# Optimization experiments

Hardware: AMD Instinct MI355X
Metric: run time of the kernel (lower is better)

Reference implementation:

```python
import jax, jax.numpy as jnp
import numpy as np

N = 8192
F_IN = 256
F_OUT = 128
ALPHA = 0.2  # leaky relu negative slope


def _leaky(x):
    return jnp.where(x >= 0, x, ALPHA * x)


def setup_inputs() -> dict:
    key = jax.random.key(0)
    ks = jax.random.split(key, 12)
    nodes = jax.random.normal(ks[0], (N, F_IN), dtype=jnp.float32)
    adj = (jax.random.uniform(ks[1], (N, N)) < 0.05).astype(jnp.float32)
    adj = jnp.maximum(adj, jnp.eye(N, dtype=jnp.float32))
    s = 0.02
    W1 = jax.random.normal(ks[2], (F_IN, F_OUT), dtype=jnp.float32) * s
    b1 = jnp.zeros((F_OUT,), jnp.float32)
    W2 = jax.random.normal(ks[3], (F_OUT, F_OUT), dtype=jnp.float32) * s
    b2 = jnp.zeros((F_OUT,), jnp.float32)
    W3 = jax.random.normal(ks[4], (F_OUT, F_OUT), dtype=jnp.float32) * s
    b3 = jnp.zeros((F_OUT,), jnp.float32)
    W4 = jax.random.normal(ks[5], (F_OUT, F_OUT), dtype=jnp.float32) * s
    b4 = jnp.zeros((F_OUT,), jnp.float32)
    a_w = jax.random.normal(ks[6], (2 * F_OUT,), dtype=jnp.float32) * s
    a_b = jnp.zeros((), jnp.float32)
    return {"nodes": nodes, "adj": adj, "W1": W1, "b1": b1, "W2": W2, "b2": b2,
            "W3": W3, "b3": b3, "W4": W4, "b4": b4, "a_w": a_w, "a_b": a_b}


def reference(nodes, adj, W1, b1, W2, b2, W3, b3, W4, b4, a_w, a_b):
    # 4-layer linear stack
    h = jax.nn.relu(nodes @ W1 + b1)
    h = jax.nn.relu(h @ W2 + b2)
    h = jax.nn.relu(h @ W3 + b3)
    h = h @ W4 + b4  # (N, F_OUT)
    # a([h_i, h_j]) is linear -> split into src/dst components instead of
    # materializing the (N, N, 2F) repeat+cat tensor; identical math.
    a1, a2 = a_w[:F_OUT], a_w[F_OUT:]
    s_src = h @ a1  # (N,)
    s_dst = h @ a2  # (N,)
    e = _leaky(s_src[:, None] + s_dst[None, :] + a_b)  # (N, N)
    e = jnp.where(adj >= 0.5, e, -jnp.inf)
    attention = jax.nn.softmax(e, axis=1)
    # dropout is identity in eval mode
    return _leaky(attention @ h)  # (N, F_OUT)
```

## Files before the change

### kernel.cpp

```cpp
#include <hip/hip_runtime.h>
#include <hip/hip_bf16.h>

#define N_NODES 8192
#define F_IN    256
#define F_OUT   128
#define BM      16
#define CHUNK   512
#define NCH     4
#define CCAP    768

typedef float f4v __attribute__((ext_vector_type(4)));
typedef unsigned int u32;

__device__ __forceinline__ float leaky(float x) { return x >= 0.f ? x : 0.2f * x; }
__device__ __forceinline__ u32 bf16rn(float a) {
  const u32 u = __float_as_uint(a);
  return (u + 0x7FFFu + ((u >> 16) & 1u)) >> 16;
}
__device__ __forceinline__ u32 packbf(float a, float b) {
  return bf16rn(a) | (bf16rn(b) << 16);
}
__device__ __forceinline__ float bflo(u32 u) { return __uint_as_float(u << 16); }
__device__ __forceinline__ float bfhi(u32 u) { return __uint_as_float(u & 0xFFFF0000u); }

__global__ __launch_bounds__(256) void mlp_fused(
    const float* __restrict__ nodes,
    const float* __restrict__ W1, const float* __restrict__ b1,
    const float* __restrict__ W2, const float* __restrict__ b2,
    const float* __restrict__ W3, const float* __restrict__ b3,
    const float* __restrict__ W4, const float* __restrict__ b4,
    const float* __restrict__ aw,
    u32* __restrict__ hb_out, float* __restrict__ ss, float* __restrict__ sd) {
  __shared__ float As[32][18];
  __shared__ float Ws[32][128];
  __shared__ float hTa[128][18];
  __shared__ float hTb[128][18];
  __shared__ float awS[2 * F_OUT];
  __shared__ float sred[2][16][16];

  const int tid = threadIdx.x;
  const int bm0 = blockIdx.x * BM;
  const int mt = tid >> 5;
  const int nt = tid & 31;

  awS[tid] = aw[tid];

  float acc[2][4] = {};

  const bool al = tid < 128;
  const int ar = tid >> 3;
  const int ac = tid & 7;
  for (int k0 = 0; k0 < F_IN; k0 += 32) {
    float4 av;
    if (al) av = *(const float4*)(nodes + (size_t)(bm0 + ar) * F_IN + k0 + ac * 4);
    float4 wv[4];
#pragma unroll
    for (int i = 0; i < 4; ++i) {
      const int kk = i * 8 + mt;
      wv[i] = *(const float4*)(W1 + (size_t)(k0 + kk) * F_OUT + nt * 4);
    }
    __syncthreads();
    if (al) {
      As[ac * 4 + 0][ar] = av.x;
      As[ac * 4 + 1][ar] = av.y;
      As[ac * 4 + 2][ar] = av.z;
      As[ac * 4 + 3][ar] = av.w;
    }
#pragma unroll
    for (int i = 0; i < 4; ++i) *(float4*)&Ws[i * 8 + mt][nt * 4] = wv[i];
    __syncthreads();
#pragma unroll
    for (int k = 0; k < 32; ++k) {
      const float2 a = *(const float2*)&As[k][mt * 2];
      const float4 w = *(const float4*)&Ws[k][nt * 4];
      acc[0][0] += a.x * w.x; acc[0][1] += a.x * w.y; acc[0][2] += a.x * w.z; acc[0][3] += a.x * w.w;
      acc[1][0] += a.y * w.x; acc[1][1] += a.y * w.y; acc[1][2] += a.y * w.z; acc[1][3] += a.y * w.w;
    }
  }
  {
    const float4 bv = *(const float4*)(b1 + nt * 4);
#pragma unroll
    for (int i = 0; i < 2; ++i) {
      hTa[nt * 4 + 0][mt * 2 + i] = fmaxf(acc[i][0] + bv.x, 0.f);
      hTa[nt * 4 + 1][mt * 2 + i] = fmaxf(acc[i][1] + bv.y, 0.f);
      hTa[nt * 4 + 2][mt * 2 + i] = fmaxf(acc[i][2] + bv.z, 0.f);
      hTa[nt * 4 + 3][mt * 2 + i] = fmaxf(acc[i][3] + bv.w, 0.f);
    }
  }

  const float* Wl[3] = {W2, W3, W4};
  const float* bl[3] = {b2, b3, b4};
  float* hin = &hTa[0][0];
  float* hout = &hTb[0][0];
  for (int l = 0; l < 3; ++l) {
#pragma unroll
    for (int i = 0; i < 2; ++i)
#pragma unroll
      for (int j = 0; j < 4; ++j) acc[i][j] = 0.f;
    for (int k0 = 0; k0 < F_OUT; k0 += 32) {
      float4 wv[4];
#pragma unroll
      for (int i = 0; i < 4; ++i) {
        const int kk = i * 8 + mt;
        wv[i] = *(const float4*)(Wl[l] + (size_t)(k0 + kk) * F_OUT + nt * 4);
      }
      __syncthreads();
#pragma unroll
      for (int i = 0; i < 4; ++i) *(float4*)&Ws[i * 8 + mt][nt * 4] = wv[i];
      __syncthreads();
#pragma unroll
      for (int k = 0; k < 32; ++k) {
        const float2 a = *(const float2*)(hin + (size_t)(k0 + k) * 18 + mt * 2);
        const float4 w = *(const float4*)&Ws[k][nt * 4];
        acc[0][0] += a.x * w.x; acc[0][1] += a.x * w.y; acc[0][2] += a.x * w.z; acc[0][3] += a.x * w.w;
        acc[1][0] += a.y * w.x; acc[1][1] += a.y * w.y; acc[1][2] += a.y * w.z; acc[1][3] += a.y * w.w;
      }
    }
    const float4 bv = *(const float4*)(bl[l] + nt * 4);
    const bool relu = (l < 2);
#pragma unroll
    for (int i = 0; i < 2; ++i) {
      float o0 = acc[i][0] + bv.x, o1 = acc[i][1] + bv.y;
      float o2 = acc[i][2] + bv.z, o3 = acc[i][3] + bv.w;
      if (relu) {
        o0 = fmaxf(o0, 0.f); o1 = fmaxf(o1, 0.f);
        o2 = fmaxf(o2, 0.f); o3 = fmaxf(o3, 0.f);
      }
      hout[(size_t)(nt * 4 + 0) * 18 + mt * 2 + i] = o0;
      hout[(size_t)(nt * 4 + 1) * 18 + mt * 2 + i] = o1;
      hout[(size_t)(nt * 4 + 2) * 18 + mt * 2 + i] = o2;
      hout[(size_t)(nt * 4 + 3) * 18 + mt * 2 + i] = o3;
    }
    float* t = hin; hin = hout; hout = t;
  }
  __syncthreads();

  {
    const int r = tid & 15;
    const int fg = tid >> 4;
    float s1 = 0.f, s2 = 0.f;
#pragma unroll
    for (int i = 0; i < 8; ++i) {
      const int f = fg * 8 + i;
      const float hv = hin[(size_t)f * 18 + r];
      s1 += hv * awS[f];
      s2 += hv * awS[F_OUT + f];
    }
    sred[0][fg][r] = s1;
    sred[1][fg][r] = s2;
  }
  {
    const int r = tid >> 4;
    const int c = tid & 15;
    const int f0 = c * 8;
    uint4 o;
    o.x = packbf(hin[(size_t)(f0 + 0) * 18 + r], hin[(size_t)(f0 + 1) * 18 + r]);
    o.y = packbf(hin[(size_t)(f0 + 2) * 18 + r], hin[(size_t)(f0 + 3) * 18 + r]);
    o.z = packbf(hin[(size_t)(f0 + 4) * 18 + r], hin[(size_t)(f0 + 5) * 18 + r]);
    o.w = packbf(hin[(size_t)(f0 + 6) * 18 + r], hin[(size_t)(f0 + 7) * 18 + r]);
    ((uint4*)hb_out)[(size_t)(bm0 + r) * 16 + c] = o;
  }
  __syncthreads();
  if (tid < 16) {
    float s1 = 0.f, s2 = 0.f;
#pragma unroll
    for (int g = 0; g < 16; ++g) { s1 += sred[0][g][tid]; s2 += sred[1][g][tid]; }
    ss[bm0 + tid] = s1;
    sd[bm0 + tid] = s2;
  }
}

__global__ __launch_bounds__(512) void attn_kernel(const float* __restrict__ adj,
                                                   const u32* __restrict__ hb,
                                                   const float* __restrict__ s_src,
                                                   const float* __restrict__ s_dst,
                                                   const float* __restrict__ ab_ptr,
                                                   float* __restrict__ out) {
  __shared__ float2 lst[2][CCAP];
  __shared__ int   cnt[NCH];
  __shared__ float accs[32][16][8];
  __shared__ float red_sum[8];

  const int tid = threadIdx.x;
  const int lane = tid & 63;
  const int wid = tid >> 6;
  const int row = blockIdx.x;
  if (tid < NCH) cnt[tid] = 0;

  const float sbase = s_src[row] + ab_ptr[0];
  const f4v* arow = (const f4v*)(adj + (size_t)row * N_NODES);
  const float4* sd4 = (const float4*)s_dst;
  const uint4* hb4 = (const uint4*)hb;
  const unsigned long long lt = (1ull << lane) - 1ull;
  const int g = tid >> 4;
  const int q = tid & 15;

  f4v av = __builtin_nontemporal_load(arow + tid);
  float4 sv = sd4[tid];

  float lsum = 0.f;
  float accv[8] = {};
  __syncthreads();

#pragma unroll
  for (int c = 0; c < NCH; ++c) {
    const f4v av_c = av;
    const float4 sv_c = sv;
    if (c + 1 < NCH) {
      av = __builtin_nontemporal_load(arow + (c + 1) * CHUNK + tid);
      sv = sd4[(c + 1) * CHUNK + tid];
    }
    const bool hx = av_c.x >= 0.5f, hy = av_c.y >= 0.5f, hz = av_c.z >= 0.5f, hw = av_c.w >= 0.5f;
    const unsigned long long m0 = __ballot(hx);
    const unsigned long long m1 = __ballot(hy);
    const unsigned long long m2 = __ballot(hz);
    const unsigned long long m3 = __ballot(hw);
    const int t0 = __popcll(m0), t1 = __popcll(m1), t2 = __popcll(m2), t3 = __popcll(m3);
    int wb = 0;
    if (lane == 0) wb = atomicAdd(&cnt[c], t0 + t1 + t2 + t3);
    wb = __shfl(wb, 0, 64);
    const int j0 = (c * CHUNK + tid) * 4;
    float2* lc = lst[c & 1];
    if (hx) {
      const int p = wb + __popcll(m0 & lt);
      if (p < CCAP) { const float w = __expf(leaky(sbase + sv_c.x)); lc[p] = make_float2(w, __int_as_float(j0)); lsum += w; }
    }
    if (hy) {
      const int p = wb + t0 + __popcll(m1 & lt);
      if (p < CCAP) { const float w = __expf(leaky(sbase + sv_c.y)); lc[p] = make_float2(w, __int_as_float(j0 + 1)); lsum += w; }
    }
    if (hz) {
      const int p = wb + t0 + t1 + __popcll(m2 & lt);
      if (p < CCAP) { const float w = __expf(leaky(sbase + sv_c.z)); lc[p] = make_float2(w, __int_as_float(j0 + 2)); lsum += w; }
    }
    if (hw) {
      const int p = wb + t0 + t1 + t2 + __popcll(m3 & lt);
      if (p < CCAP) { const float w = __expf(leaky(sbase + sv_c.w)); lc[p] = make_float2(w, __int_as_float(j0 + 3)); lsum += w; }
    }
    __syncthreads();
    const int n = min(cnt[c], CCAP);
#pragma unroll 2
    for (int p = g; p < n; p += 32) {
      const float2 pr = lc[p];
      const uint4 hv = hb4[(size_t)__float_as_int(pr.y) * 16 + q];
      accv[0] += pr.x * bflo(hv.x); accv[1] += pr.x * bfhi(hv.x);
      accv[2] += pr.x * bflo(hv.y); accv[3] += pr.x * bfhi(hv.y);
      accv[4] += pr.x * bflo(hv.z); accv[5] += pr.x * bfhi(hv.z);
      accv[6] += pr.x * bflo(hv.w); accv[7] += pr.x * bfhi(hv.w);
    }
  }

#pragma unroll
  for (int o = 1; o < 64; o <<= 1) lsum += __shfl_xor(lsum, o, 64);
  if (lane == 0) red_sum[wid] = lsum;
#pragma unroll
  for (int e = 0; e < 8; ++e) accs[g][q][e] = accv[e];
  __syncthreads();
  if (tid < 128) {
    const int q2 = tid >> 3, e = tid & 7;
    float s = 0.f;
#pragma unroll
    for (int g2 = 0; g2 < 32; ++g2) s += accs[g2][q2][e];
    float ws_ = 0.f;
#pragma unroll
    for (int wv = 0; wv < 8; ++wv) ws_ += red_sum[wv];
    out[(size_t)row * F_OUT + tid] = leaky(s / ws_);
  }
}

extern "C" void kernel_launch(void* const* d_in, const int* in_sizes, int n_in,
                              void* d_out, int out_size, void* d_ws, size_t ws_size,
                              hipStream_t stream) {
  const float* nodes = (const float*)d_in[0];
  const float* adj   = (const float*)d_in[1];
  const float* W1    = (const float*)d_in[2];
  const float* b1    = (const float*)d_in[3];
  const float* W2    = (const float*)d_in[4];
  const float* b2    = (const float*)d_in[5];
  const float* W3    = (const float*)d_in[6];
  const float* b3    = (const float*)d_in[7];
  const float* W4    = (const float*)d_in[8];
  const float* b4    = (const float*)d_in[9];
  const float* aw    = (const float*)d_in[10];
  const float* ab    = (const float*)d_in[11];
  float* out = (float*)d_out;

  u32*  hb = (u32*)d_ws;
  float* ss = (float*)((char*)d_ws + (size_t)N_NODES * F_OUT * 2);
  float* sd = ss + N_NODES;

  mlp_fused<<<N_NODES / BM, 256, 0, stream>>>(nodes, W1, b1, W2, b2, W3, b3,
                                              W4, b4, aw, hb, ss, sd);
  attn_kernel<<<N_NODES, 512, 0, stream>>>(adj, hb, ss, sd, ab, out);
}
```

Before: 465.9 us.

## Restructure MLP kernel into per-wave 8-row tiles with register-streamed weights

Rewrites the fused MLP kernel so that each wave independently owns 8 rows. Each lane computes 2 output columns, with weights read straight from global memory into registers through double buffering. Activations stay in per-wave LDS with no block-level __syncthreads, and the attention score dot products are reduced with wave shuffles. This removes the block-wide barriers and the shared weight staging. In exchange every wave re-reads the weight matrices from global or L2, and per-wave LDS use rises to 16KB. The attention kernel, which dominates runtime, is unchanged.

After: 469.4 us. No clear change (+0.8%).

```diff
diff --git a/kernel.cpp b/kernel.cpp
--- a/kernel.cpp
+++ b/kernel.cpp
@@ -4,7 +4,6 @@
 #define N_NODES 8192
 #define F_IN    256
 #define F_OUT   128
-#define BM      16
 #define CHUNK   512
 #define NCH     4
 #define CCAP    768
@@ -22,6 +21,45 @@
 }
 __device__ __forceinline__ float bflo(u32 u) { return __uint_as_float(u << 16); }
 __device__ __forceinline__ float bfhi(u32 u) { return __uint_as_float(u & 0xFFFF0000u); }
+
+#define WAVE_LDS (8 * 256 + 8 * 128 + 8 * 128)
+
+__device__ __forceinline__ void mlp_step4(const float* hbase, int stride, int k0,
+                                          const float2 w[4], float acc[8][2]) {
+#pragma unroll
+  for (int r = 0; r < 8; ++r) {
+    const float4 h4 = *(const float4*)(hbase + r * stride + k0);
+    acc[r][0] += h4.x * w[0].x; acc[r][1] += h4.x * w[0].y;
+    acc[r][0] += h4.y * w[1].x; acc[r][1] += h4.y * w[1].y;
+    acc[r][0] += h4.z * w[2].x; acc[r][1] += h4.z * w[2].y;
+    acc[r][0] += h4.w * w[3].x; acc[r][1] += h4.w * w[3].y;
+  }
+}
+
+template <int K, int STRIDE>
+__device__ __forceinline__ void mlp_layer(const float* __restrict__ W, int n0,
+                                          const float* hbase, float acc[8][2]) {
+#pragma unroll
+  for (int r = 0; r < 8; ++r) { acc[r][0] = 0.f; acc[r][1] = 0.f; }
+  float2 wA[4], wB[4];
+#pragma unroll
+  for (int kk = 0; kk < 4; ++kk)
+    wA[kk] = *(const float2*)(W + (size_t)kk * F_OUT + n0);
+#pragma unroll 1
+  for (int k8 = 0; k8 < K / 8; ++k8) {
+    const int kb = k8 * 8;
+#pragma unroll
+    for (int kk = 0; kk < 4; ++kk)
+      wB[kk] = *(const float2*)(W + (size_t)(kb + 4 + kk) * F_OUT + n0);
+    mlp_step4(hbase, STRIDE, kb, wA, acc);
+    if (k8 + 1 < K / 8) {
+#pragma unroll
+      for (int kk = 0; kk < 4; ++kk)
+        wA[kk] = *(const float2*)(W + (size_t)(kb + 8 + kk) * F_OUT + n0);
+    }
+    mlp_step4(hbase, STRIDE, kb + 4, wB, acc);
+  }
+}
 
 __global__ __launch_bounds__(256) void mlp_fused(
     const float* __restrict__ nodes,
@@ -31,142 +69,73 @@
     const float* __restrict__ W4, const float* __restrict__ b4,
     const float* __restrict__ aw,
     u32* __restrict__ hb_out, float* __restrict__ ss, float* __restrict__ sd) {
-  __shared__ float As[32][18];
-  __shared__ float Ws[32][128];
-  __shared__ float hTa[128][18];
-  __shared__ float hTb[128][18];
-  __shared__ float awS[2 * F_OUT];
-  __shared__ float sred[2][16][16];
+  __shared__ float lds[4][WAVE_LDS];
 
   const int tid = threadIdx.x;
-  const int bm0 = blockIdx.x * BM;
-  const int mt = tid >> 5;
-  const int nt = tid & 31;
-
-  awS[tid] = aw[tid];
-
-  float acc[2][4] = {};
-
-  const bool al = tid < 128;
-  const int ar = tid >> 3;
-  const int ac = tid & 7;
-  for (int k0 = 0; k0 < F_IN; k0 += 32) {
-    float4 av;
-    if (al) av = *(const float4*)(nodes + (size_t)(bm0 + ar) * F_IN + k0 + ac * 4);
-    float4 wv[4];
-#pragma unroll
-    for (int i = 0; i < 4; ++i) {
-      const int kk = i * 8 + mt;
-      wv[i] = *(const float4*)(W1 + (size_t)(k0 + kk) * F_OUT + nt * 4);
-    }
-    __syncthreads();
-    if (al) {
-      As[ac * 4 + 0][ar] = av.x;
-      As[ac * 4 + 1][ar] = av.y;
-      As[ac * 4 + 2][ar] = av.z;
-      As[ac * 4 + 3][ar] = av.w;
-    }
-#pragma unroll
-    for (int i = 0; i < 4; ++i) *(float4*)&Ws[i * 8 + mt][nt * 4] = wv[i];
-    __syncthreads();
-#pragma unroll
-    for (int k = 0; k < 32; ++k) {
-      const float2 a = *(const float2*)&As[k][mt * 2];
-      const float4 w = *(const float4*)&Ws[k][nt * 4];
-      acc[0][0] += a.x * w.x; acc[0][1] += a.x * w.y; acc[0][2] += a.x * w.z; acc[0][3] += a.x * w.w;
-      acc[1][0] += a.y * w.x; acc[1][1] += a.y * w.y; acc[1][2] += a.y * w.z; acc[1][3] += a.y * w.w;
-    }
-  }
-  {
-    const float4 bv = *(const float4*)(b1 + nt * 4);
-#pragma unroll
-    for (int i = 0; i < 2; ++i) {
-      hTa[nt * 4 + 0][mt * 2 + i] = fmaxf(acc[i][0] + bv.x, 0.f);
-      hTa[nt * 4 + 1][mt * 2 + i] = fmaxf(acc[i][1] + bv.y, 0.f);
-      hTa[nt * 4 + 2][mt * 2 + i] = fmaxf(acc[i][2] + bv.z, 0.f);
-      hTa[nt * 4 + 3][mt * 2 + i] = fmaxf(acc[i][3] + bv.w, 0.f);
-    }
-  }
-
-  const float* Wl[3] = {W2, W3, W4};
-  const float* bl[3] = {b2, b3, b4};
-  float* hin = &hTa[0][0];
-  float* hout = &hTb[0][0];
-  for (int l = 0; l < 3; ++l) {
-#pragma unroll
-    for (int i = 0; i < 2; ++i)
-#pragma unroll
-      for (int j = 0; j < 4; ++j) acc[i][j] = 0.f;
-    for (int k0 = 0; k0 < F_OUT; k0 += 32) {
-      float4 wv[4];
-#pragma unroll
-      for (int i = 0; i < 4; ++i) {
-        const int kk = i * 8 + mt;
-        wv[i] = *(const float4*)(Wl[l] + (size_t)(k0 + kk) * F_OUT + nt * 4);
-      }
-      __syncthreads();
-#pragma unroll
-      for (int i = 0; i < 4; ++i) *(float4*)&Ws[i * 8 + mt][nt * 4] = wv[i];
-      __syncthreads();
-#pragma unroll
-      for (int k = 0; k < 32; ++k) {
-        const float2 a = *(const float2*)(hin + (size_t)(k0 + k) * 18 + mt * 2);
-        const float4 w = *(const float4*)&Ws[k][nt * 4];
-        acc[0][0] += a.x * w.x; acc[0][1] += a.x * w.y; acc[0][2] += a.x * w.z; acc[0][3] += a.x * w.w;
-        acc[1][0] += a.y * w.x; acc[1][1] += a.y * w.y; acc[1][2] += a.y * w.z; acc[1][3] += a.y * w.w;
-      }
-    }
-    const float4 bv = *(const float4*)(bl[l] + nt * 4);
-    const bool relu = (l < 2);
-#pragma unroll
-    for (int i = 0; i < 2; ++i) {
-      float o0 = acc[i][0] + bv.x, o1 = acc[i][1] + bv.y;
-      float o2 = acc[i][2] + bv.z, o3 = acc[i][3] + bv.w;
-      if (relu) {
-        o0 = fmaxf(o0, 0.f); o1 = fmaxf(o1, 0.f);
-        o2 = fmaxf(o2, 0.f); o3 = fmaxf(o3, 0.f);
-      }
-      hout[(size_t)(nt * 4 + 0) * 18 + mt * 2 + i] = o0;
-      hout[(size_t)(nt * 4 + 1) * 18 + mt * 2 + i] = o1;
-      hout[(size_t)(nt * 4 + 2) * 18 + mt * 2 + i] = o2;
-      hout[(size_t)(nt * 4 + 3) * 18 + mt * 2 + i] = o3;
-    }
-    float* t = hin; hin = hout; hout = t;
-  }
-  __syncthreads();
-
-  {
-    const int r = tid & 15;
-    const int fg = tid >> 4;
-    float s1 = 0.f, s2 = 0.f;
-#pragma unroll
-    for (int i = 0; i < 8; ++i) {
-      const int f = fg * 8 + i;
-      const float hv = hin[(size_t)f * 18 + r];
-      s1 += hv * awS[f];
-      s2 += hv * awS[F_OUT + f];
-    }
-    sred[0][fg][r] = s1;
-    sred[1][fg][r] = s2;
-  }
-  {
-    const int r = tid >> 4;
-    const int c = tid & 15;
-    const int f0 = c * 8;
-    uint4 o;
-    o.x = packbf(hin[(size_t)(f0 + 0) * 18 + r], hin[(size_t)(f0 + 1) * 18 + r]);
-    o.y = packbf(hin[(size_t)(f0 + 2) * 18 + r], hin[(size_t)(f0 + 3) * 18 + r]);
-    o.z = packbf(hin[(size_t)(f0 + 4) * 18 + r], hin[(size_t)(f0 + 5) * 18 + r]);
-    o.w = packbf(hin[(size_t)(f0 + 6) * 18 + r], hin[(size_t)(f0 + 7) * 18 + r]);
-    ((uint4*)hb_out)[(size_t)(bm0 + r) * 16 + c] = o;
-  }
-  __syncthreads();
-  if (tid < 16) {
-    float s1 = 0.f, s2 = 0.f;
-#pragma unroll
-    for (int g = 0; g < 16; ++g) { s1 += sred[0][g][tid]; s2 += sred[1][g][tid]; }
-    ss[bm0 + tid] = s1;
-    sd[bm0 + tid] = s2;
+  const int w = tid >> 6;
+  const int l = tid & 63;
+  const int row0 = blockIdx.x * 32 + w * 8;
+  const int n0 = 2 * l;
+
+  float* A  = &lds[w][0];
+  float* h1 = &lds[w][2048];
+  float* h2 = &lds[w][2048 + 1024];
+
+#pragma unroll
+  for (int r = 0; r < 8; ++r) {
+    const float4 v = *(const float4*)(nodes + (size_t)(row0 + r) * F_IN + l * 4);
+    *(float4*)&A[r * 256 + l * 4] = v;
+  }
+
+  float acc[8][2];
+
+  mlp_layer<256, 256>(W1, n0, A, acc);
+  {
+    const float2 bv = *(const float2*)(b1 + n0);
+#pragma unroll
+    for (int r = 0; r < 8; ++r) {
+      float2 o = {fmaxf(acc[r][0] + bv.x, 0.f), fmaxf(acc[r][1] + bv.y, 0.f)};
+      *(float2*)&h1[r * 128 + n0] = o;
+    }
+  }
+  mlp_layer<128, 128>(W2, n0, h1, acc);
+  {
+    const float2 bv = *(const float2*)(b2 + n0);
+#pragma unroll
+    for (int r = 0; r < 8; ++r) {
+      float2 o = {fmaxf(acc[r][0] + bv.x, 0.f), fmaxf(acc[r][1] + bv.y, 0.f)};
+      *(float2*)&h2[r * 128 + n0] = o;
+    }
+  }
+  mlp_layer<128, 128>(W3, n0, h2, acc);
+  {
+    const float2 bv = *(const float2*)(b3 + n0);
+#pragma unroll
+    for (int r = 0; r < 8; ++r) {
+      float2 o = {fmaxf(acc[r][0] + bv.x, 0.f), fmaxf(acc[r][1] + bv.y, 0.f)};
+      *(float2*)&h1[r * 128 + n0] = o;
+    }
+  }
+  mlp_layer<128, 128>(W4, n0, h1, acc);
+  {
+    const float2 bv = *(const float2*)(b4 + n0);
+#pragma unroll
+    for (int r = 0; r < 8; ++r) { acc[r][0] += bv.x; acc[r][1] += bv.y; }
+  }
+
+  const float2 a1v = *(const float2*)(aw + n0);
+  const float2 a2v = *(const float2*)(aw + F_OUT + n0);
+#pragma unroll
+  for (int r = 0; r < 8; ++r) {
+    hb_out[(size_t)(row0 + r) * 64 + l] = packbf(acc[r][0], acc[r][1]);
+    float s1 = acc[r][0] * a1v.x + acc[r][1] * a1v.y;
+    float s2 = acc[r][0] * a2v.x + acc[r][1] * a2v.y;
+#pragma unroll
+    for (int o = 1; o < 64; o <<= 1) {
+      s1 += __shfl_xor(s1, o, 64);
+      s2 += __shfl_xor(s2, o, 64);
+    }
+    if (l == 0) { ss[row0 + r] = s1; sd[row0 + r] = s2; }
   }
 }
 
@@ -289,7 +258,7 @@
   float* ss = (float*)((char*)d_ws + (size_t)N_NODES * F_OUT * 2);
   float* sd = ss + N_NODES;
 
-  mlp_fused<<<N_NODES / BM, 256, 0, stream>>>(nodes, W1, b1, W2, b2, W3, b3,
+  mlp_fused<<<N_NODES / 32, 256, 0, stream>>>(nodes, W1, b1, W2, b2, W3, b3,
                                               W4, b4, aw, hb, ss, sd);
   attn_kernel<<<N_NODES, 512, 0, stream>>>(adj, hb, ss, sd, ab, out);
 }
```
